# Kernel tuning notes

Hardware: AMD Instinct MI355X
Metric: run time of the kernel (lower is better)

## Reference

```python
import jax, jax.numpy as jnp
import numpy as np

B, H, W = 4, 512, 512
N = 262144
CIN, COUT = 64, 64
NUM_INS = 16
RATES = (1, 3, 5)
EPS = 1e-5


def _subm_conv(feats, idx_map, bidx, y, x, seg, d_pt, w, b, same_ins):
    # Submanifold 3x3 conv on sparse sites: for each active point, gather the
    # 8 neighbors at offsets scaled by the (per-point) dilation; a neighbor
    # contributes only if it is an active site (and, for the per-instance
    # branches, belongs to the same instance).
    out = jnp.zeros((feats.shape[0], w.shape[-1]), feats.dtype)
    k = 0
    for ky in (-1, 0, 1):
        for kx in (-1, 0, 1):
            ny = y + ky * d_pt
            nx = x + kx * d_pt
            inb = (ny >= 0) & (ny < H) & (nx >= 0) & (nx < W)
            nbr = idx_map[bidx, jnp.clip(ny, 0, H - 1), jnp.clip(nx, 0, W - 1)]
            valid = inb & (nbr >= 0)
            if same_ins:
                valid = valid & (seg[nbr] == seg)
            f = jnp.where(valid[:, None], feats[nbr], 0.0)  # masked gather
            out = out + f @ w[k]
            k += 1
    return out + b


def _ins_norm(xf, seg):
    # InstanceNorm1d per instance segment: normalize each channel over the
    # instance's points (biased variance, no affine, eps=1e-5).
    cnt = jax.ops.segment_sum(jnp.ones((xf.shape[0],), xf.dtype), seg, NUM_INS)
    s = jax.ops.segment_sum(xf, seg, NUM_INS)
    s2 = jax.ops.segment_sum(xf * xf, seg, NUM_INS)
    mean = s / cnt[:, None]
    var = s2 / cnt[:, None] - mean * mean
    return (xf - mean[seg]) * jax.lax.rsqrt(var[seg] + EPS)


def _dilation_per_point(y, x, seg, rate):
    # d_i = max(1, ceil(max(h_ratio, w_ratio) * dilation_max)) per instance.
    ymin = jax.ops.segment_min(y, seg, NUM_INS)
    ymax = jax.ops.segment_max(y, seg, NUM_INS)
    xmin = jax.ops.segment_min(x, seg, NUM_INS)
    xmax = jax.ops.segment_max(x, seg, NUM_INS)
    hr = (ymax - ymin).astype(jnp.float32) / H
    wr = (xmax - xmin).astype(jnp.float32) / W
    d = jnp.maximum(1, jnp.ceil(jnp.maximum(hr, wr) * rate)).astype(jnp.int32)
    return d[seg]


def setup_inputs() -> dict:
    key = jax.random.key(0)
    ks = jax.random.split(key, 12)
    # unique active sites on the B x H x W grid (required for a valid index map)
    flat = jax.random.permutation(ks[0], B * H * W)[:N]
    b = (flat // (H * W)).astype(jnp.int32)
    rem = flat % (H * W)
    y = (rem // W).astype(jnp.int32)
    x = (rem % W).astype(jnp.int32)
    indices = jnp.stack([b, y, x], axis=1)
    # instance ids, sorted so points are grouped per instance (matches the
    # per-instance concat ordering of the original module)
    ins_indices_batch = jnp.sort(
        jax.random.randint(ks[1], (N,), 0, NUM_INS)).astype(jnp.int32)
    features = jax.random.normal(ks[2], (N, CIN), jnp.float32)
    wscale = 1.0 / np.sqrt(9 * CIN)
    inp = {
        "features": features,
        "indices": indices,
        "ins_indices_batch": ins_indices_batch,
        "w1": jax.random.normal(ks[3], (9, CIN, COUT), jnp.float32) * wscale,
        "b1": jax.random.normal(ks[4], (COUT,), jnp.float32) * 0.02,
        "w2": jax.random.normal(ks[5], (9, CIN, COUT), jnp.float32) * wscale,
        "b2": jax.random.normal(ks[6], (COUT,), jnp.float32) * 0.02,
        "w3": jax.random.normal(ks[7], (9, CIN, COUT), jnp.float32) * wscale,
        "b3": jax.random.normal(ks[8], (COUT,), jnp.float32) * 0.02,
        "wf": jax.random.normal(ks[9], (9, CIN + 3 * COUT, COUT), jnp.float32)
              * (1.0 / np.sqrt(9 * (CIN + 3 * COUT))),
        "bf": jax.random.normal(ks[10], (COUT,), jnp.float32) * 0.02,
    }
    return inp


def reference(features, indices, ins_indices_batch, w1, b1, w2, b2, w3, b3, wf, bf):
    bidx, y, x = indices[:, 0], indices[:, 1], indices[:, 2]
    seg = ins_indices_batch
    # dense map from (b,y,x) -> row index (-1 = inactive)
    idx_map = jnp.full((B, H, W), -1, jnp.int32).at[bidx, y, x].set(
        jnp.arange(N, dtype=jnp.int32))
    branches = []
    for w_, b_, rate in ((w1, b1, RATES[0]), (w2, b2, RATES[1]), (w3, b3, RATES[2])):
        d_pt = _dilation_per_point(y, x, seg, rate)
        h = _subm_conv(features, idx_map, bidx, y, x, seg, d_pt, w_, b_, True)
        h = jax.nn.relu(_ins_norm(h, seg))
        branches.append(h)
    cat = jnp.concatenate([features] + branches, axis=1)  # [N, CIN+3*COUT]
    ones = jnp.ones((N,), jnp.int32)
    return _subm_conv(cat, idx_map, bidx, y, x, seg, ones, wf, bf, False)
```

## Files before the change

### kernel.cpp

```cpp
#include <hip/hip_runtime.h>
#include <hip/hip_bf16.h>
#include <stdint.h>

#define N_PTS   262144
#define H_DIM   512
#define W_DIM   512
#define N_SEG   16
#define EPS_V   1e-5f

typedef __bf16 bf16_t;
typedef __bf16 bf16x8 __attribute__((ext_vector_type(8)));
typedef float  f32x4  __attribute__((ext_vector_type(4)));

__device__ __forceinline__ void gl_lds16(const bf16_t* g, bf16_t* l) {
  __builtin_amdgcn_global_load_lds(
      (const __attribute__((address_space(1))) unsigned int*)g,
      (__attribute__((address_space(3))) unsigned int*)l, 16, 0, 0);
}


__global__ void init_kernel(int* cnt, int* ymin, int* ymax, int* xmin, int* xmax,
                            float* sums, float* sumsq, int* hist) {
  int t = threadIdx.x;
  if (t < N_SEG) {
    cnt[t] = 0;
    ymin[t] = 0x7fffffff; ymax[t] = (int)0x80000000;
    xmin[t] = 0x7fffffff; xmax[t] = (int)0x80000000;
  }
  for (int i = t; i < 3 * 1024; i += 256) { sums[i] = 0.f; sumsq[i] = 0.f; }
  if (hist) for (int i = t; i < 4096; i += 256) hist[i] = 0;
}

__global__ void scatter_kernel(const int* __restrict__ indices,
                               const int* __restrict__ seg,
                               int* __restrict__ idx_map,
                               int* __restrict__ cnt,
                               int* __restrict__ ymin, int* __restrict__ ymax,
                               int* __restrict__ xmin, int* __restrict__ xmax,
                               int* __restrict__ hist) {
  __shared__ int lc[N_SEG], ly0[N_SEG], ly1[N_SEG], lx0[N_SEG], lx1[N_SEG];
  int tid = threadIdx.x;
  if (tid < N_SEG) {
    lc[tid] = 0;
    ly0[tid] = 0x7fffffff; ly1[tid] = (int)0x80000000;
    lx0[tid] = 0x7fffffff; lx1[tid] = (int)0x80000000;
  }
  __syncthreads();
  int i = blockIdx.x * 256 + tid;
  int b = indices[i * 3], y = indices[i * 3 + 1], x = indices[i * 3 + 2];
  int s = seg[i];
  idx_map[(b * H_DIM + y) * W_DIM + x] = (s << 18) | i;
  atomicAdd(&lc[s], 1);
  atomicMin(&ly0[s], y); atomicMax(&ly1[s], y);
  atomicMin(&lx0[s], x); atomicMax(&lx1[s], x);
  if (hist) {
    int key = (b << 10) | ((y >> 4) << 5) | (x >> 4);
    atomicAdd(&hist[key], 1);
  }
  __syncthreads();
  if (tid < N_SEG && lc[tid] > 0) {
    atomicAdd(&cnt[tid], lc[tid]);
    atomicMin(&ymin[tid], ly0[tid]); atomicMax(&ymax[tid], ly1[tid]);
    atomicMin(&xmin[tid], lx0[tid]); atomicMax(&xmax[tid], lx1[tid]);
  }
}

__global__ void scan_kernel(const int* __restrict__ hist, int* __restrict__ cursor) {
  __shared__ int s[256];
  int t = threadIdx.x;
  int base = t * 16;
  int loc[16];
  int acc = 0;
#pragma unroll
  for (int j = 0; j < 16; ++j) { loc[j] = acc; acc += hist[base + j]; }
  s[t] = acc;
  __syncthreads();
  for (int o = 1; o < 256; o <<= 1) {
    int v = (t >= o) ? s[t - o] : 0;
    __syncthreads();
    s[t] += v;
    __syncthreads();
  }
  int pre = (t == 0) ? 0 : s[t - 1];
#pragma unroll
  for (int j = 0; j < 16; ++j) cursor[base + j] = pre + loc[j];
}

__global__ void rank_kernel(const int* __restrict__ indices,
                            int* __restrict__ cursor, int* __restrict__ ord) {
  int i = blockIdx.x * 256 + threadIdx.x;
  int b = indices[i * 3], y = indices[i * 3 + 1], x = indices[i * 3 + 2];
  int key = (b << 10) | ((y >> 4) << 5) | (x >> 4);
  int pos = atomicAdd(&cursor[key], 1);
  ord[pos] = i;
}

__global__ void dilation_kernel(const int* ymin, const int* ymax,
                                const int* xmin, const int* xmax,
                                const int* cnt, int* dseg) {
  int t = threadIdx.x;
  if (t < 48) {
    int r = t >> 4, s = t & 15;
    int rate = (r == 0) ? 1 : (r == 1) ? 3 : 5;
    int d = 1;
    if (cnt[s] > 0) {
      float hr = (float)(ymax[s] - ymin[s]) * (1.0f / H_DIM);
      float wr = (float)(xmax[s] - xmin[s]) * (1.0f / W_DIM);
      d = (int)ceilf(fmaxf(hr, wr) * (float)rate);
      if (d < 1) d = 1;
    }
    dseg[t] = d;
  }
}

__global__ void convert_kernel(const float4* __restrict__ in, bf16_t* __restrict__ dst,
                               int stride) {
  int i = blockIdx.x * 256 + threadIdx.x;
  int pt = i >> 4, g = i & 15;
  float4 v = in[i];
  union { bf16_t h[4]; uint2 u; } o;
  o.h[0] = (bf16_t)v.x; o.h[1] = (bf16_t)v.y;
  o.h[2] = (bf16_t)v.z; o.h[3] = (bf16_t)v.w;
  *(uint2*)(dst + (size_t)pt * stride + g * 4) = o.u;
}

__global__ void repack_kernel(const float* __restrict__ w1, const float* __restrict__ w2,
                              const float* __restrict__ w3, const float* __restrict__ wf,
                              bf16_t* __restrict__ wfrag) {
  int e = blockIdx.x * 256 + threadIdx.x;
  if (e < 110592) {
    int s = e / 36864, rem = e % 36864;
    int k = rem >> 12, r2 = rem & 4095;
    int kk = r2 >> 11, r3 = r2 & 2047;
    int cot = r3 >> 9, r4 = r3 & 511;
    int lane = r4 >> 3, j = r4 & 7;
    int c  = kk * 32 + (lane >> 4) * 8 + j;
    int co = cot * 16 + (lane & 15);
    const float* w = (s == 0) ? w1 : (s == 1) ? w2 : w3;
    wfrag[e] = (bf16_t)w[k * 4096 + c * 64 + co];
  } else {
    int ef = e - 110592;
    int k = ef >> 14, r2 = ef & 16383;
    int kk8 = r2 >> 11, r3 = r2 & 2047;
    int cot = r3 >> 9, r4 = r3 & 511;
    int lane = r4 >> 3, j = r4 & 7;
    int c  = kk8 * 32 + (lane >> 4) * 8 + j;
    int co = cot * 16 + (lane & 15);
    wfrag[e] = (bf16_t)wf[k * 16384 + c * 64 + co];
  }
}

#define MF(ar, wr, i, j) \
  acc[i][j] = __builtin_amdgcn_mfma_f32_16x16x32_bf16(ar, wr, acc[i][j], 0, 0, 0)
#define MF16(A0, A1, A2, A3, W0, W1, W2, W3) \
  MF(A0, W0, 0, 0); MF(A0, W1, 0, 1); MF(A0, W2, 0, 2); MF(A0, W3, 0, 3); \
  MF(A1, W0, 1, 0); MF(A1, W1, 1, 1); MF(A1, W2, 1, 2); MF(A1, W3, 1, 3); \
  MF(A2, W0, 2, 0); MF(A2, W1, 2, 1); MF(A2, W2, 2, 2); MF(A2, W3, 2, 3); \
  MF(A3, W0, 3, 0); MF(A3, W1, 3, 1); MF(A3, W2, 3, 2); MF(A3, W3, 3, 3)

template <int KK, int MODE>
__launch_bounds__(256, 3)
__global__ void conv_mfma(const bf16_t* __restrict__ A, int astride,
                          const bf16_t* __restrict__ wfrag, int wkstride,
                          const int* __restrict__ indices,
                          const int* __restrict__ seg,
                          const int* __restrict__ idx_map,
                          const int* __restrict__ dseg,
                          const int* __restrict__ ord,
                          float* __restrict__ outf,
                          bf16_t* __restrict__ outh, int hstride, int hoff,
                          const float* __restrict__ bias) {
  constexpr int WELEM = (KK == 8) ? 8192 : 4096;
  constexpr int SWEEPS = (KK == 8) ? 4 : 2;
  __shared__ int s_nbr[9 * 256];
  __shared__ int s_pt[256];
  __shared__ bf16_t s_w[2][WELEM];
  const int tid = threadIdx.x;
  int bid = blockIdx.x;
  if (ord) bid = (bid & 7) * ((int)gridDim.x >> 3) + (bid >> 3);
  const int pt0 = bid * 256;

  {
    int pt = ord ? ord[pt0 + tid] : (pt0 + tid);
    s_pt[tid] = pt;
    int b = indices[pt * 3], y = indices[pt * 3 + 1], x = indices[pt * 3 + 2];
    int sg = 0, d = 1;
    if (MODE == 0) { sg = seg[pt]; d = dseg[sg]; }
#pragma unroll
    for (int k = 0; k < 9; ++k) {
      int ky = (k / 3) - 1, kx = (k % 3) - 1;
      int ny = y + ky * d, nx = x + kx * d;
      int nbr = N_PTS;
      if (ny >= 0 && ny < H_DIM && nx >= 0 && nx < W_DIM) {
        int v = idx_map[(b * H_DIM + ny) * W_DIM + nx];
        if (v >= 0) {
          if (MODE == 0) nbr = ((v >> 18) == sg) ? (v & 0x3FFFF) : N_PTS;
          else           nbr = v & 0x3FFFF;
        }
      }
      s_nbr[k * 256 + tid] = nbr;
    }
  }

  auto stage = [&](int ph, int buf) {
    const bf16_t* src;
    if constexpr (KK == 8) src = wfrag + (size_t)(ph >> 1) * wkstride + (ph & 1) * 8192;
    else                   src = wfrag + (size_t)ph * wkstride;
#pragma unroll
    for (int s = 0; s < SWEEPS; ++s) {
      int off = s * 2048 + tid * 8;
      gl_lds16(src + off, &s_w[buf][off]);
    }
  };

  stage(0, 0);
  __syncthreads();

  const int lane = tid & 63;
  const int wv = tid >> 6;
  const int m = lane & 15;
  const int quad = lane >> 4;
  const int rbase = wv * 64 + m;

  f32x4 acc[4][4];
#pragma unroll
  for (int rt = 0; rt < 4; ++rt)
#pragma unroll
    for (int c = 0; c < 4; ++c) {
      acc[rt][c][0] = 0.f; acc[rt][c][1] = 0.f;
      acc[rt][c][2] = 0.f; acc[rt][c][3] = 0.f;
    }

  if constexpr (KK == 2) {
    for (int k = 0; k < 9; ++k) {
      const int cur = k & 1;
      if (k < 8) stage(k + 1, cur ^ 1);
      const int* sn = s_nbr + k * 256 + rbase;
      const bf16_t* a0p = A + (size_t)sn[0]  * astride + quad * 8;
      const bf16_t* a1p = A + (size_t)sn[16] * astride + quad * 8;
      const bf16_t* a2p = A + (size_t)sn[32] * astride + quad * 8;
      const bf16_t* a3p = A + (size_t)sn[48] * astride + quad * 8;
      bf16x8 a00 = *(const bf16x8*)(a0p), a01 = *(const bf16x8*)(a0p + 32);
      bf16x8 a10 = *(const bf16x8*)(a1p), a11 = *(const bf16x8*)(a1p + 32);
      bf16x8 a20 = *(const bf16x8*)(a2p), a21 = *(const bf16x8*)(a2p + 32);
      bf16x8 a30 = *(const bf16x8*)(a3p), a31 = *(const bf16x8*)(a3p + 32);
      const bf16_t* wl = &s_w[cur][lane * 8];
      bf16x8 w00 = *(const bf16x8*)(wl +    0), w01 = *(const bf16x8*)(wl +  512);
      bf16x8 w02 = *(const bf16x8*)(wl + 1024), w03 = *(const bf16x8*)(wl + 1536);
      bf16x8 w10 = *(const bf16x8*)(wl + 2048), w11 = *(const bf16x8*)(wl + 2560);
      bf16x8 w12 = *(const bf16x8*)(wl + 3072), w13 = *(const bf16x8*)(wl + 3584);
      MF16(a00, a10, a20, a30, w00, w01, w02, w03);
      MF16(a01, a11, a21, a31, w10, w11, w12, w13);
      __syncthreads();
    }
  } else {
    for (int h = 0; h < 18; ++h) {
      const int cur = h & 1;
      if (h < 17) stage(h + 1, cur ^ 1);
      const int k = h >> 1;
      const int colb = (h & 1) * 128;
      const int* sn = s_nbr + k * 256 + rbase;
      const bf16_t* a0p = A + (size_t)sn[0]  * astride + quad * 8 + colb;
      const bf16_t* a1p = A + (size_t)sn[16] * astride + quad * 8 + colb;
      const bf16_t* a2p = A + (size_t)sn[32] * astride + quad * 8 + colb;
      const bf16_t* a3p = A + (size_t)sn[48] * astride + quad * 8 + colb;
#pragma unroll
      for (int kp = 0; kp < 2; ++kp) {
        const int cb = kp * 64;
        bf16x8 a00 = *(const bf16x8*)(a0p + cb), a01 = *(const bf16x8*)(a0p + cb + 32);
        bf16x8 a10 = *(const bf16x8*)(a1p + cb), a11 = *(const bf16x8*)(a1p + cb + 32);
        bf16x8 a20 = *(const bf16x8*)(a2p + cb), a21 = *(const bf16x8*)(a2p + cb + 32);
        bf16x8 a30 = *(const bf16x8*)(a3p + cb), a31 = *(const bf16x8*)(a3p + cb + 32);
        const bf16_t* wl = &s_w[cur][kp * 4096 + lane * 8];
        bf16x8 w00 = *(const bf16x8*)(wl +    0), w01 = *(const bf16x8*)(wl +  512);
        bf16x8 w02 = *(const bf16x8*)(wl + 1024), w03 = *(const bf16x8*)(wl + 1536);
        bf16x8 w10 = *(const bf16x8*)(wl + 2048), w11 = *(const bf16x8*)(wl + 2560);
        bf16x8 w12 = *(const bf16x8*)(wl + 3072), w13 = *(const bf16x8*)(wl + 3584);
        MF16(a00, a10, a20, a30, w00, w01, w02, w03);
        MF16(a01, a11, a21, a31, w10, w11, w12, w13);
      }
      __syncthreads();
    }
  }

#pragma unroll
  for (int rt = 0; rt < 4; ++rt) {
#pragma unroll
    for (int reg = 0; reg < 4; ++reg) {
      int r = wv * 64 + rt * 16 + quad * 4 + reg;
      int pt = s_pt[r];
#pragma unroll
      for (int cot = 0; cot < 4; ++cot) {
        int col = cot * 16 + m;
        float v = acc[rt][cot][reg];
        if (MODE == 0)      outh[(size_t)pt * hstride + hoff + col] = (bf16_t)v;
        else if (MODE == 1) outf[(size_t)pt * 64 + col] = v + bias[col];
        else                outf[(size_t)pt * 64 + col] += v;
      }
    }
  }
}

__global__ void stats_kernel(const bf16_t* __restrict__ h, int stride, int off,
                             const int* __restrict__ seg,
                             float* __restrict__ sums, float* __restrict__ sumsq) {
  int tid = threadIdx.x;
  int co = tid & 63, pr = tid >> 6;
  int base = blockIdx.x * 1024;
  float s = 0.f, s2 = 0.f;
  int cur = seg[base];
  for (int i = pr; i < 1024; i += 4) {
    int pt = base + i;
    int sg = seg[pt];
    float v = (float)h[(size_t)pt * stride + off + co];
    if (sg != cur) {
      atomicAdd(&sums[cur * 64 + co], s);
      atomicAdd(&sumsq[cur * 64 + co], s2);
      s = 0.f; s2 = 0.f; cur = sg;
    }
    s += v; s2 += v * v;
  }
  atomicAdd(&sums[cur * 64 + co], s);
  atomicAdd(&sumsq[cur * 64 + co], s2);
}

__global__ void params_kernel(const int* __restrict__ cnt, const float* __restrict__ sums,
                              const float* __restrict__ sumsq,
                              float* __restrict__ pA, float* __restrict__ pB) {
  int t = blockIdx.x * 256 + threadIdx.x;
  if (t < 1024) {
    int sgi = t >> 6;
    float c = (float)cnt[sgi];
    float a = 0.f, b = 0.f;
    if (c > 0.f) {
      float mean = sums[t] / c;
      float var = sumsq[t] / c - mean * mean;
      float inv = rsqrtf(var + EPS_V);
      a = inv; b = -mean * inv;
    }
    pA[t] = a; pB[t] = b;
  }
}

__global__ void norm_kernel(bf16_t* __restrict__ h, int stride, int off,
                            const int* __restrict__ seg,
                            const float* __restrict__ pA, const float* __restrict__ pB) {
  int i = blockIdx.x * 256 + threadIdx.x;
  int pt = i >> 4;
  int cg = (i & 15) * 4;
  int sg = seg[pt];
  bf16_t* p = h + (size_t)pt * stride + off + cg;
  union { bf16_t hh[4]; uint2 u; } v;
  v.u = *(uint2*)p;
#pragma unroll
  for (int j = 0; j < 4; ++j) {
    float f = (float)v.hh[j] * pA[sg * 64 + cg + j] + pB[sg * 64 + cg + j];
    v.hh[j] = (bf16_t)fmaxf(f, 0.f);
  }
  *(uint2*)p = v.u;
}

extern "C" void kernel_launch(void* const* d_in, const int* in_sizes, int n_in,
                              void* d_out, int out_size, void* d_ws, size_t ws_size,
                              hipStream_t stream) {
  const float* feats   = (const float*)d_in[0];
  const int*   indices = (const int*)d_in[1];
  const int*   seg     = (const int*)d_in[2];
  const float* w1 = (const float*)d_in[3];
  const float* w2 = (const float*)d_in[5];
  const float* w3 = (const float*)d_in[7];
  const float* wf = (const float*)d_in[9];
  const float* bf_ = (const float*)d_in[10];
  float* out = (float*)d_out;

  char* ws = (char*)d_ws;
  const bool sorted = (ws_size >= 140200000ull);
  const bool fused  = sorted || (ws_size >= 139000000ull);

  int* idx_map = (int*)(ws + 0);
  hipMemsetAsync(idx_map, 0xFF, 4194304, stream);

  if (fused) {
    bf16_t* cat   = (bf16_t*)(ws + 4194304);
    bf16_t* wfrag = (bf16_t*)(ws + 138412544);
    float*  stats = (float*)(ws + 138928640);
    int* cnt  = (int*)stats;
    int* ymin = (int*)(stats + 16);
    int* ymax = (int*)(stats + 32);
    int* xmin = (int*)(stats + 48);
    int* xmax = (int*)(stats + 64);
    int* dseg = (int*)(stats + 80);
    float* sums  = stats + 128;
    float* sumsq = stats + 3200;
    float* pA    = stats + 6272;
    float* pB    = stats + 9344;
    int* hist   = sorted ? (int*)(stats + 12416) : nullptr;
    int* cursor = sorted ? hist + 4096 : nullptr;
    int* ord    = sorted ? hist + 8192 : nullptr;

    hipMemsetAsync(cat + (size_t)N_PTS * 256, 0, 512, stream);
    init_kernel<<<1, 256, 0, stream>>>(cnt, ymin, ymax, xmin, xmax, sums, sumsq, hist);
    scatter_kernel<<<N_PTS / 256, 256, 0, stream>>>(indices, seg, idx_map, cnt, ymin, ymax, xmin, xmax, hist);
    dilation_kernel<<<1, 64, 0, stream>>>(ymin, ymax, xmin, xmax, cnt, dseg);
    if (sorted) {
      scan_kernel<<<1, 256, 0, stream>>>(hist, cursor);
      rank_kernel<<<N_PTS / 256, 256, 0, stream>>>(indices, cursor, ord);
    }
    convert_kernel<<<16384, 256, 0, stream>>>((const float4*)feats, cat, 256);
    repack_kernel<<<1008, 256, 0, stream>>>(w1, w2, w3, wf, wfrag);

    for (int r = 0; r < 3; ++r) {
      conv_mfma<2, 0><<<1024, 256, 0, stream>>>(cat, 256, wfrag + (size_t)r * 36864, 4096,
                                                indices, seg, idx_map, dseg + r * 16, ord,
                                                nullptr, cat, 256, (r + 1) * 64, nullptr);
      stats_kernel<<<256, 256, 0, stream>>>(cat, 256, (r + 1) * 64, seg,
                                            sums + r * 1024, sumsq + r * 1024);
      params_kernel<<<4, 256, 0, stream>>>(cnt, sums + r * 1024, sumsq + r * 1024,
                                           pA + r * 1024, pB + r * 1024);
      norm_kernel<<<16384, 256, 0, stream>>>(cat, 256, (r + 1) * 64, seg,
                                             pA + r * 1024, pB + r * 1024);
    }
    conv_mfma<8, 1><<<1024, 256, 0, stream>>>(cat, 256, wfrag + 110592, 16384,
                                              indices, seg, idx_map, nullptr, ord,
                                              out, nullptr, 0, 0, bf_);
  } else {
    bf16_t* feats_bf = (bf16_t*)(ws + 4194304);
    bf16_t* h_bf     = (bf16_t*)(ws + 37748864);
    bf16_t* wfrag    = (bf16_t*)(ws + 71303424);
    float*  stats    = (float*)(ws + 71819520);
    int* cnt  = (int*)stats;
    int* ymin = (int*)(stats + 16);
    int* ymax = (int*)(stats + 32);
    int* xmin = (int*)(stats + 48);
    int* xmax = (int*)(stats + 64);
    int* dseg = (int*)(stats + 80);
    float* sums  = stats + 128;
    float* sumsq = stats + 3200;
    float* pA    = stats + 6272;
    float* pB    = stats + 9344;

    hipMemsetAsync(feats_bf + (size_t)N_PTS * 64, 0, 128, stream);
    hipMemsetAsync(h_bf + (size_t)N_PTS * 64, 0, 128, stream);
    init_kernel<<<1, 256, 0, stream>>>(cnt, ymin, ymax, xmin, xmax, sums, sumsq, nullptr);
    scatter_kernel<<<N_PTS / 256, 256, 0, stream>>>(indices, seg, idx_map, cnt, ymin, ymax, xmin, xmax, nullptr);
    dilation_kernel<<<1, 64, 0, stream>>>(ymin, ymax, xmin, xmax, cnt, dseg);
    convert_kernel<<<16384, 256, 0, stream>>>((const float4*)feats, feats_bf, 64);
    repack_kernel<<<1008, 256, 0, stream>>>(w1, w2, w3, wf, wfrag);

    conv_mfma<2, 1><<<1024, 256, 0, stream>>>(feats_bf, 64, wfrag + 110592, 16384,
                                              indices, seg, idx_map, nullptr, nullptr,
                                              out, nullptr, 0, 0, bf_);
    for (int r = 0; r < 3; ++r) {
      conv_mfma<2, 0><<<1024, 256, 0, stream>>>(feats_bf, 64, wfrag + (size_t)r * 36864, 4096,
                                                indices, seg, idx_map, dseg + r * 16, nullptr,
                                                nullptr, h_bf, 64, 0, nullptr);
      stats_kernel<<<256, 256, 0, stream>>>(h_bf, 64, 0, seg, sums + r * 1024, sumsq + r * 1024);
      params_kernel<<<4, 256, 0, stream>>>(cnt, sums + r * 1024, sumsq + r * 1024,
                                           pA + r * 1024, pB + r * 1024);
      norm_kernel<<<16384, 256, 0, stream>>>(h_bf, 64, 0, seg, pA + r * 1024, pB + r * 1024);
      conv_mfma<2, 2><<<1024, 256, 0, stream>>>(h_bf, 64, wfrag + 110592 + (size_t)(r + 1) * 4096, 16384,
                                                indices, seg, idx_map, nullptr, nullptr,
                                                out, nullptr, 0, 0, nullptr);
    }
  }
}
```

Baseline: 705.9 us.

## Physically reorder points into spatial tile order and gather in-tile neighbors from LDS

Rank points by spatial tile, then write features, a packed metadata array and an idx_map holding sorted positions, so all later kernels work in tile-sorted row order. A new conv kernel stages each block's own 256 rows into swizzled LDS and reads neighbors that fall inside the block from LDS instead of global memory. Stats and norm kernels read the segment from the packed metadata. The final output is scattered back to original order through ord. This needs a larger workspace threshold to enable and adds extra LDS use, which lowers occupancy to 2 blocks per CU.

```diff
diff --git a/kernel.cpp b/kernel.cpp
--- a/kernel.cpp
+++ b/kernel.cpp
@@ -87,12 +87,17 @@
 }
 
 __global__ void rank_kernel(const int* __restrict__ indices,
-                            int* __restrict__ cursor, int* __restrict__ ord) {
+                            const int* __restrict__ seg,
+                            int* __restrict__ cursor, int* __restrict__ ord,
+                            int* __restrict__ meta, int* __restrict__ idx_map) {
   int i = blockIdx.x * 256 + threadIdx.x;
   int b = indices[i * 3], y = indices[i * 3 + 1], x = indices[i * 3 + 2];
   int key = (b << 10) | ((y >> 4) << 5) | (x >> 4);
   int pos = atomicAdd(&cursor[key], 1);
+  int s = seg[i];
   ord[pos] = i;
+  meta[pos] = (s << 20) | (b << 18) | (y << 9) | x;
+  idx_map[(b * H_DIM + y) * W_DIM + x] = (s << 18) | pos;
 }
 
 __global__ void dilation_kernel(const int* ymin, const int* ymax,
@@ -114,10 +119,11 @@
 }
 
 __global__ void convert_kernel(const float4* __restrict__ in, bf16_t* __restrict__ dst,
-                               int stride) {
+                               int stride, const int* __restrict__ ord) {
   int i = blockIdx.x * 256 + threadIdx.x;
   int pt = i >> 4, g = i & 15;
-  float4 v = in[i];
+  int sp = ord ? ord[pt] : pt;
+  float4 v = in[(size_t)sp * 16 + g];
   union { bf16_t h[4]; uint2 u; } o;
   o.h[0] = (bf16_t)v.x; o.h[1] = (bf16_t)v.y;
   o.h[2] = (bf16_t)v.z; o.h[3] = (bf16_t)v.w;
@@ -152,11 +158,180 @@
 
 #define MF(ar, wr, i, j) \
   acc[i][j] = __builtin_amdgcn_mfma_f32_16x16x32_bf16(ar, wr, acc[i][j], 0, 0, 0)
-#define MF16(A0, A1, A2, A3, W0, W1, W2, W3) \
-  MF(A0, W0, 0, 0); MF(A0, W1, 0, 1); MF(A0, W2, 0, 2); MF(A0, W3, 0, 3); \
-  MF(A1, W0, 1, 0); MF(A1, W1, 1, 1); MF(A1, W2, 1, 2); MF(A1, W3, 1, 3); \
-  MF(A2, W0, 2, 0); MF(A2, W1, 2, 1); MF(A2, W2, 2, 2); MF(A2, W3, 2, 3); \
-  MF(A3, W0, 3, 0); MF(A3, W1, 3, 1); MF(A3, W2, 3, 2); MF(A3, W3, 3, 3)
+
+template <int KK, int MODE>
+__launch_bounds__(256, 2)
+__global__ void conv_sorted(const bf16_t* __restrict__ A,
+                            const bf16_t* __restrict__ wfrag, int wkstride,
+                            const int* __restrict__ meta,
+                            const int* __restrict__ idx_map,
+                            const int* __restrict__ dseg,
+                            const int* __restrict__ ord,
+                            float* __restrict__ outf,
+                            bf16_t* __restrict__ outh, int hoff,
+                            const float* __restrict__ bias) {
+  __shared__ __align__(16) bf16_t s_a[256 * 64];
+  __shared__ __align__(16) bf16_t s_w[2][4096];
+  __shared__ int s_nbr[9 * 256];
+  __shared__ int s_pt[256];
+  const int tid = threadIdx.x;
+  int bid = blockIdx.x;
+  bid = (bid & 7) * ((int)gridDim.x >> 3) + (bid >> 3);
+  const int pt0 = bid * 256;
+
+  {
+    int mt = meta[pt0 + tid];
+    if (MODE == 1) s_pt[tid] = ord[pt0 + tid];
+    int sg = mt >> 20;
+    int b = (mt >> 18) & 3, y = (mt >> 9) & 511, x = mt & 511;
+    int d = (MODE == 0) ? dseg[sg] : 1;
+#pragma unroll
+    for (int k = 0; k < 9; ++k) {
+      int ky = (k / 3) - 1, kx = (k % 3) - 1;
+      int ny = y + ky * d, nx = x + kx * d;
+      int e = N_PTS;
+      if (ny >= 0 && ny < H_DIM && nx >= 0 && nx < W_DIM) {
+        int v = idx_map[(b * H_DIM + ny) * W_DIM + nx];
+        if (v >= 0) {
+          int pos2 = v & 0x3FFFF;
+          if (MODE == 0) { if ((v >> 18) == sg) e = pos2; }
+          else e = pos2;
+        }
+      }
+      unsigned lo = (unsigned)(e - pt0);
+      s_nbr[k * 256 + tid] = (lo < 256u) ? -(int)(lo + 1) : e;
+    }
+  }
+
+  const int lane = tid & 63;
+  const int wv = tid >> 6;
+  const int m = lane & 15;
+  const int quad = lane >> 4;
+  const int rb = wv * 64 + m;
+
+  float b4[4];
+  if (MODE == 1) {
+#pragma unroll
+    for (int cot = 0; cot < 4; ++cot) b4[cot] = bias[cot * 16 + m];
+  }
+
+  auto stageA = [&](int q) {
+#pragma unroll
+    for (int s = 0; s < 8; ++s) {
+      int ch = s * 256 + tid;
+      int r = ch >> 3, p = ch & 7;
+      int ps = p ^ (r & 7);
+      gl_lds16(A + (size_t)(pt0 + r) * 256 + q * 64 + ps * 8, &s_a[ch * 8]);
+    }
+  };
+  auto stageW = [&](int k, int q, int buf) {
+    const bf16_t* src = wfrag + (size_t)k * wkstride + q * 4096;
+#pragma unroll
+    for (int s = 0; s < 2; ++s) {
+      int off = s * 2048 + tid * 8;
+      gl_lds16(src + off, &s_w[buf][off]);
+    }
+  };
+
+  f32x4 acc[4][4];
+#pragma unroll
+  for (int rt = 0; rt < 4; ++rt)
+#pragma unroll
+    for (int c = 0; c < 4; ++c) {
+      acc[rt][c][0] = 0.f; acc[rt][c][1] = 0.f;
+      acc[rt][c][2] = 0.f; acc[rt][c][3] = 0.f;
+    }
+
+  constexpr int NQ = (KK == 8) ? 4 : 1;
+  for (int q = 0; q < NQ; ++q) {
+    __syncthreads();
+    stageA(q);
+    stageW(0, q, 0);
+    __syncthreads();
+    int buf = 0;
+    for (int k = 0; k < 9; ++k) {
+      if (k < 8) stageW(k + 1, q, buf ^ 1);
+      const int* sn = s_nbr + k * 256;
+#pragma unroll
+      for (int rt = 0; rt < 4; ++rt) {
+        int e = sn[rb + rt * 16];
+        bool loc = e < 0;
+        int slot = loc ? (-e - 1) : 0;
+        int grow = loc ? N_PTS : e;
+        const bf16_t* gp = A + (size_t)grow * 256 + q * 64 + quad * 8;
+        bf16x8 g0 = *(const bf16x8*)(gp);
+        bf16x8 g1 = *(const bf16x8*)(gp + 32);
+        int sw = slot & 7;
+        bf16x8 l0 = *(const bf16x8*)&s_a[slot * 64 + ((quad ^ sw) << 3)];
+        bf16x8 l1 = *(const bf16x8*)&s_a[slot * 64 + (((4 + quad) ^ sw) << 3)];
+        bf16x8 a0 = loc ? l0 : g0;
+        bf16x8 a1 = loc ? l1 : g1;
+        const bf16_t* wl = &s_w[buf][lane * 8];
+        MF(a0, *(const bf16x8*)(wl +    0), rt, 0);
+        MF(a0, *(const bf16x8*)(wl +  512), rt, 1);
+        MF(a0, *(const bf16x8*)(wl + 1024), rt, 2);
+        MF(a0, *(const bf16x8*)(wl + 1536), rt, 3);
+        MF(a1, *(const bf16x8*)(wl + 2048), rt, 0);
+        MF(a1, *(const bf16x8*)(wl + 2560), rt, 1);
+        MF(a1, *(const bf16x8*)(wl + 3072), rt, 2);
+        MF(a1, *(const bf16x8*)(wl + 3584), rt, 3);
+      }
+      __syncthreads();
+      buf ^= 1;
+    }
+  }
+
+  if (MODE == 0) {
+#pragma unroll
+    for (int rt = 0; rt < 4; ++rt)
+#pragma unroll
+      for (int reg = 0; reg < 4; ++reg) {
+        int row = wv * 64 + rt * 16 + quad * 4 + reg;
+#pragma unroll
+        for (int cot = 0; cot < 4; ++cot) {
+          int col = cot * 16 + m;
+          int p = col >> 3;
+          s_a[row * 64 + (((p ^ (row & 7)) << 3) | (col & 7))] = (bf16_t)acc[rt][cot][reg];
+        }
+      }
+    __syncthreads();
+#pragma unroll
+    for (int s = 0; s < 8; ++s) {
+      int g = s * 256 + tid;
+      int r = g >> 3, p = g & 7;
+      uint4 v = *(const uint4*)&s_a[r * 64 + ((p ^ (r & 7)) << 3)];
+      *(uint4*)(outh + (size_t)(pt0 + r) * 256 + hoff + p * 8) = v;
+    }
+  } else {
+    float* s_af = (float*)s_a;
+#pragma unroll
+    for (int hh = 0; hh < 2; ++hh) {
+      if (hh) __syncthreads();
+#pragma unroll
+      for (int rt = 0; rt < 4; ++rt)
+#pragma unroll
+        for (int reg = 0; reg < 4; ++reg) {
+          int row = wv * 64 + rt * 16 + quad * 4 + reg;
+#pragma unroll
+          for (int c2 = 0; c2 < 2; ++c2) {
+            int cot = hh * 2 + c2;
+            int col32 = c2 * 16 + m;
+            int p = col32 >> 2;
+            s_af[row * 32 + (((p ^ (row & 7)) << 2) | (col32 & 3))] =
+                acc[rt][cot][reg] + b4[cot];
+          }
+        }
+      __syncthreads();
+#pragma unroll
+      for (int s = 0; s < 8; ++s) {
+        int g = s * 256 + tid;
+        int r = g >> 3, p = g & 7;
+        float4 v = *(const float4*)&s_af[r * 32 + ((p ^ (r & 7)) << 2)];
+        *(float4*)(outf + (size_t)s_pt[r] * 64 + hh * 32 + p * 4) = v;
+      }
+    }
+  }
+}
 
 template <int KK, int MODE>
 __launch_bounds__(256, 3)
@@ -166,23 +341,18 @@
                           const int* __restrict__ seg,
                           const int* __restrict__ idx_map,
                           const int* __restrict__ dseg,
-                          const int* __restrict__ ord,
                           float* __restrict__ outf,
                           bf16_t* __restrict__ outh, int hstride, int hoff,
                           const float* __restrict__ bias) {
   constexpr int WELEM = (KK == 8) ? 8192 : 4096;
   constexpr int SWEEPS = (KK == 8) ? 4 : 2;
   __shared__ int s_nbr[9 * 256];
-  __shared__ int s_pt[256];
-  __shared__ bf16_t s_w[2][WELEM];
+  __shared__ __align__(16) bf16_t s_w[2][WELEM];
   const int tid = threadIdx.x;
-  int bid = blockIdx.x;
-  if (ord) bid = (bid & 7) * ((int)gridDim.x >> 3) + (bid >> 3);
-  const int pt0 = bid * 256;
+  const int pt0 = blockIdx.x * 256;
 
   {
-    int pt = ord ? ord[pt0 + tid] : (pt0 + tid);
-    s_pt[tid] = pt;
+    int pt = pt0 + tid;
     int b = indices[pt * 3], y = indices[pt * 3 + 1], x = indices[pt * 3 + 2];
     int sg = 0, d = 1;
     if (MODE == 0) { sg = seg[pt]; d = dseg[sg]; }
@@ -230,6 +400,12 @@
       acc[rt][c][0] = 0.f; acc[rt][c][1] = 0.f;
       acc[rt][c][2] = 0.f; acc[rt][c][3] = 0.f;
     }
+
+#define MF16X(A0, A1, A2, A3, W0, W1, W2, W3) \
+  MF(A0, W0, 0, 0); MF(A0, W1, 0, 1); MF(A0, W2, 0, 2); MF(A0, W3, 0, 3); \
+  MF(A1, W0, 1, 0); MF(A1, W1, 1, 1); MF(A1, W2, 1, 2); MF(A1, W3, 1, 3); \
+  MF(A2, W0, 2, 0); MF(A2, W1, 2, 1); MF(A2, W2, 2, 2); MF(A2, W3, 2, 3); \
+  MF(A3, W0, 3, 0); MF(A3, W1, 3, 1); MF(A3, W2, 3, 2); MF(A3, W3, 3, 3)
 
   if constexpr (KK == 2) {
     for (int k = 0; k < 9; ++k) {
@@ -249,8 +425,8 @@
       bf16x8 w02 = *(const bf16x8*)(wl + 1024), w03 = *(const bf16x8*)(wl + 1536);
       bf16x8 w10 = *(const bf16x8*)(wl + 2048), w11 = *(const bf16x8*)(wl + 2560);
       bf16x8 w12 = *(const bf16x8*)(wl + 3072), w13 = *(const bf16x8*)(wl + 3584);
-      MF16(a00, a10, a20, a30, w00, w01, w02, w03);
-      MF16(a01, a11, a21, a31, w10, w11, w12, w13);
+      MF16X(a00, a10, a20, a30, w00, w01, w02, w03);
+      MF16X(a01, a11, a21, a31, w10, w11, w12, w13);
       __syncthreads();
     }
   } else {
@@ -276,8 +452,8 @@
         bf16x8 w02 = *(const bf16x8*)(wl + 1024), w03 = *(const bf16x8*)(wl + 1536);
         bf16x8 w10 = *(const bf16x8*)(wl + 2048), w11 = *(const bf16x8*)(wl + 2560);
         bf16x8 w12 = *(const bf16x8*)(wl + 3072), w13 = *(const bf16x8*)(wl + 3584);
-        MF16(a00, a10, a20, a30, w00, w01, w02, w03);
-        MF16(a01, a11, a21, a31, w10, w11, w12, w13);
+        MF16X(a00, a10, a20, a30, w00, w01, w02, w03);
+        MF16X(a01, a11, a21, a31, w10, w11, w12, w13);
       }
       __syncthreads();
     }
@@ -287,8 +463,7 @@
   for (int rt = 0; rt < 4; ++rt) {
 #pragma unroll
     for (int reg = 0; reg < 4; ++reg) {
-      int r = wv * 64 + rt * 16 + quad * 4 + reg;
-      int pt = s_pt[r];
+      int pt = pt0 + wv * 64 + rt * 16 + quad * 4 + reg;
 #pragma unroll
       for (int cot = 0; cot < 4; ++cot) {
         int col = cot * 16 + m;
@@ -324,6 +499,29 @@
   atomicAdd(&sumsq[cur * 64 + co], s2);
 }
 
+__global__ void stats_sorted(const bf16_t* __restrict__ h, int off,
+                             const int* __restrict__ meta,
+                             float* __restrict__ sums, float* __restrict__ sumsq) {
+  __shared__ float bs[N_SEG * 64], bq[N_SEG * 64];
+  int tid = threadIdx.x;
+  for (int i = tid; i < N_SEG * 64; i += 256) { bs[i] = 0.f; bq[i] = 0.f; }
+  __syncthreads();
+  int co = tid & 63, pr = tid >> 6;
+  int base = blockIdx.x * 1024;
+  for (int i = pr; i < 1024; i += 4) {
+    int pt = base + i;
+    int sg = meta[pt] >> 20;
+    float v = (float)h[(size_t)pt * 256 + off + co];
+    atomicAdd(&bs[sg * 64 + co], v);
+    atomicAdd(&bq[sg * 64 + co], v * v);
+  }
+  __syncthreads();
+  for (int i = tid; i < N_SEG * 64; i += 256) {
+    if (bs[i] != 0.f) atomicAdd(&sums[i], bs[i]);
+    if (bq[i] != 0.f) atomicAdd(&sumsq[i], bq[i]);
+  }
+}
+
 __global__ void params_kernel(const int* __restrict__ cnt, const float* __restrict__ sums,
                               const float* __restrict__ sumsq,
                               float* __restrict__ pA, float* __restrict__ pB) {
@@ -360,6 +558,24 @@
   *(uint2*)p = v.u;
 }
 
+__global__ void norm_sorted(bf16_t* __restrict__ h, int off,
+                            const int* __restrict__ meta,
+                            const float* __restrict__ pA, const float* __restrict__ pB) {
+  int i = blockIdx.x * 256 + threadIdx.x;
+  int pt = i >> 4;
+  int cg = (i & 15) * 4;
+  int sg = meta[pt] >> 20;
+  bf16_t* p = h + (size_t)pt * 256 + off + cg;
+  union { bf16_t hh[4]; uint2 u; } v;
+  v.u = *(uint2*)p;
+#pragma unroll
+  for (int j = 0; j < 4; ++j) {
+    float f = (float)v.hh[j] * pA[sg * 64 + cg + j] + pB[sg * 64 + cg + j];
+    v.hh[j] = (bf16_t)fmaxf(f, 0.f);
+  }
+  *(uint2*)p = v.u;
+}
+
 extern "C" void kernel_launch(void* const* d_in, const int* in_sizes, int n_in,
                               void* d_out, int out_size, void* d_ws, size_t ws_size,
                               hipStream_t stream) {
@@ -374,8 +590,8 @@
   float* out = (float*)d_out;
 
   char* ws = (char*)d_ws;
-  const bool sorted = (ws_size >= 140200000ull);
-  const bool fused  = sorted || (ws_size >= 139000000ull);
+  const bool t2 = (ws_size >= 141200000ull);
+  const bool fused = t2 || (ws_size >= 139000000ull);
 
   int* idx_map = (int*)(ws + 0);
   hipMemsetAsync(idx_map, 0xFF, 4194304, stream);
@@ -394,35 +610,53 @@
     float* sumsq = stats + 3200;
     float* pA    = stats + 6272;
     float* pB    = stats + 9344;
-    int* hist   = sorted ? (int*)(stats + 12416) : nullptr;
-    int* cursor = sorted ? hist + 4096 : nullptr;
-    int* ord    = sorted ? hist + 8192 : nullptr;
+    int* hist   = t2 ? (int*)(ws + 138978304) : nullptr;
+    int* cursor = t2 ? (int*)(ws + 138994688) : nullptr;
+    int* ord    = t2 ? (int*)(ws + 139011072) : nullptr;
+    int* meta   = t2 ? (int*)(ws + 140059648) : nullptr;
 
     hipMemsetAsync(cat + (size_t)N_PTS * 256, 0, 512, stream);
     init_kernel<<<1, 256, 0, stream>>>(cnt, ymin, ymax, xmin, xmax, sums, sumsq, hist);
     scatter_kernel<<<N_PTS / 256, 256, 0, stream>>>(indices, seg, idx_map, cnt, ymin, ymax, xmin, xmax, hist);
     dilation_kernel<<<1, 64, 0, stream>>>(ymin, ymax, xmin, xmax, cnt, dseg);
-    if (sorted) {
+    if (t2) {
       scan_kernel<<<1, 256, 0, stream>>>(hist, cursor);
-      rank_kernel<<<N_PTS / 256, 256, 0, stream>>>(indices, cursor, ord);
-    }
-    convert_kernel<<<16384, 256, 0, stream>>>((const float4*)feats, cat, 256);
+      rank_kernel<<<N_PTS / 256, 256, 0, stream>>>(indices, seg, cursor, ord, meta, idx_map);
+    }
+    convert_kernel<<<16384, 256, 0, stream>>>((const float4*)feats, cat, 256, ord);
     repack_kernel<<<1008, 256, 0, stream>>>(w1, w2, w3, wf, wfrag);
 
-    for (int r = 0; r < 3; ++r) {
-      conv_mfma<2, 0><<<1024, 256, 0, stream>>>(cat, 256, wfrag + (size_t)r * 36864, 4096,
-                                                indices, seg, idx_map, dseg + r * 16, ord,
-                                                nullptr, cat, 256, (r + 1) * 64, nullptr);
-      stats_kernel<<<256, 256, 0, stream>>>(cat, 256, (r + 1) * 64, seg,
-                                            sums + r * 1024, sumsq + r * 1024);
-      params_kernel<<<4, 256, 0, stream>>>(cnt, sums + r * 1024, sumsq + r * 1024,
-                                           pA + r * 1024, pB + r * 1024);
-      norm_kernel<<<16384, 256, 0, stream>>>(cat, 256, (r + 1) * 64, seg,
+    if (t2) {
+      for (int r = 0; r < 3; ++r) {
+        conv_sorted<2, 0><<<1024, 256, 0, stream>>>(cat, wfrag + (size_t)r * 36864, 4096,
+                                                    meta, idx_map, dseg + r * 16, nullptr,
+                                                    nullptr, cat, (r + 1) * 64, nullptr);
+        stats_sorted<<<256, 256, 0, stream>>>(cat, (r + 1) * 64, meta,
+                                              sums + r * 1024, sumsq + r * 1024);
+        params_kernel<<<4, 256, 0, stream>>>(cnt, sums + r * 1024, sumsq + r * 1024,
                                              pA + r * 1024, pB + r * 1024);
-    }
-    conv_mfma<8, 1><<<1024, 256, 0, stream>>>(cat, 256, wfrag + 110592, 16384,
-                                              indices, seg, idx_map, nullptr, ord,
-                                              out, nullptr, 0, 0, bf_);
+        norm_sorted<<<16384, 256, 0, stream>>>(cat, (r + 1) * 64, meta,
+                                               pA + r * 1024, pB + r * 1024);
+      }
+      conv_sorted<8, 1><<<1024, 256, 0, stream>>>(cat, wfrag + 110592, 16384,
+                                                  meta, idx_map, nullptr, ord,
+                                                  out, nullptr, 0, bf_);
+    } else {
+      for (int r = 0; r < 3; ++r) {
+        conv_mfma<2, 0><<<1024, 256, 0, stream>>>(cat, 256, wfrag + (size_t)r * 36864, 4096,
+                                                  indices, seg, idx_map, dseg + r * 16,
+                                                  nullptr, cat, 256, (r + 1) * 64, nullptr);
+        stats_kernel<<<256, 256, 0, stream>>>(cat, 256, (r + 1) * 64, seg,
+                                              sums + r * 1024, sumsq + r * 1024);
+        params_kernel<<<4, 256, 0, stream>>>(cnt, sums + r * 1024, sumsq + r * 1024,
+                                             pA + r * 1024, pB + r * 1024);
+        norm_kernel<<<16384, 256, 0, stream>>>(cat, 256, (r + 1) * 64, seg,
+                                               pA + r * 1024, pB + r * 1024);
+      }
+      conv_mfma<8, 1><<<1024, 256, 0, stream>>>(cat, 256, wfrag + 110592, 16384,
+                                                indices, seg, idx_map, nullptr,
+                                                out, nullptr, 0, 0, bf_);
+    }
   } else {
     bf16_t* feats_bf = (bf16_t*)(ws + 4194304);
     bf16_t* h_bf     = (bf16_t*)(ws + 37748864);
@@ -444,22 +678,22 @@
     init_kernel<<<1, 256, 0, stream>>>(cnt, ymin, ymax, xmin, xmax, sums, sumsq, nullptr);
     scatter_kernel<<<N_PTS / 256, 256, 0, stream>>>(indices, seg, idx_map, cnt, ymin, ymax, xmin, xmax, nullptr);
     dilation_kernel<<<1, 64, 0, stream>>>(ymin, ymax, xmin, xmax, cnt, dseg);
-    convert_kernel<<<16384, 256, 0, stream>>>((const float4*)feats, feats_bf, 64);
+    convert_kernel<<<16384, 256, 0, stream>>>((const float4*)feats, feats_bf, 64, nullptr);
     repack_kernel<<<1008, 256, 0, stream>>>(w1, w2, w3, wf, wfrag);
 
     conv_mfma<2, 1><<<1024, 256, 0, stream>>>(feats_bf, 64, wfrag + 110592, 16384,
-                                              indices, seg, idx_map, nullptr, nullptr,
+                                              indices, seg, idx_map, nullptr,
                                               out, nullptr, 0, 0, bf_);
     for (int r = 0; r < 3; ++r) {
       conv_mfma<2, 0><<<1024, 256, 0, stream>>>(feats_bf, 64, wfrag + (size_t)r * 36864, 4096,
-                                                indices, seg, idx_map, dseg + r * 16, nullptr,
+                                                indices, seg, idx_map, dseg + r * 16,
                                                 nullptr, h_bf, 64, 0, nullptr);
       stats_kernel<<<256, 256, 0, stream>>>(h_bf, 64, 0, seg, sums + r * 1024, sumsq + r * 1024);
       params_kernel<<<4, 256, 0, stream>>>(cnt, sums + r * 1024, sumsq + r * 1024,
                                            pA + r * 1024, pB + r * 1024);
       norm_kernel<<<16384, 256, 0, stream>>>(h_bf, 64, 0, seg, pA + r * 1024, pB + r * 1024);
       conv_mfma<2, 2><<<1024, 256, 0, stream>>>(h_bf, 64, wfrag + 110592 + (size_t)(r + 1) * 4096, 16384,
-                                                indices, seg, idx_map, nullptr, nullptr,
+                                                indices, seg, idx_map, nullptr,
                                                 out, nullptr, 0, 0, nullptr);
     }
   }
```

New measurement: 1.019 ms. 44.4% more time.
